# Kernel tuning notes

Measured on AMD Instinct MI355X. Metric: run time of the kernel, lower is better.

Reference implementation:

```python
import jax, jax.numpy as jnp
import numpy as np

C_LIGHT = 3e8
SPATIAL, CROP = 128, 128
BIN_LEN, WALL_SIZE, SAMPLING_COEFF, CYCLES = 0.01, 2.0, 2.0, 5
B, D, T = 1, 2, 96


def waveconvparam(bin_resolution, virtual_wavelength, cycles):
    # Gaussian-windowed virtual cos/sin illumination wave (phasor-field heterodyne).
    s_z = bin_resolution * C_LIGHT
    samples = int(round(cycles * virtual_wavelength / s_z))
    num_cycles = samples * s_z / virtual_wavelength
    sigma = 0.3
    grids_k = np.arange(samples, dtype=np.float64) + 1.0
    sin_wave_k = np.sin(2.0 * np.pi * (num_cycles * grids_k) / samples)
    cos_wave_k = np.cos(2.0 * np.pi * (num_cycles * grids_k) / samples)
    n = np.arange(samples, dtype=np.float64) - (samples - 1) / 2.0
    window = np.exp(-0.5 * (n / (sigma * samples)) ** 2)
    return (cos_wave_k * window).astype(np.float32), (sin_wave_k * window).astype(np.float32)


def definePsf(sptial_grid, temprol_grid, slope):
    # Standard LCT light-cone PSF (O'Toole et al.).
    N, M = sptial_grid, temprol_grid
    x = np.linspace(-1.0, 1.0, 2 * N)
    y = np.linspace(-1.0, 1.0, 2 * N)
    z = np.linspace(0.0, 2.0, 2 * M)
    gz, gy, gx = np.meshgrid(z, y, x, indexing='ij')  # (2M, 2N, 2N)
    psf = np.abs(((4.0 * slope) ** 2) * (gx ** 2 + gy ** 2) - gz)
    psf = (psf == psf.min(axis=0, keepdims=True)).astype(np.float64)
    psf = psf / np.sum(psf[:, N, N])
    psf = psf / np.linalg.norm(psf.ravel())
    psf = np.roll(np.roll(psf, N, axis=1), N, axis=2)
    return psf


def resamplingOperator(M):
    mtx = np.zeros((M * M, M), dtype=np.float64)
    x = np.arange(1, M * M + 1)
    mtx[x - 1, np.ceil(np.sqrt(x)).astype(np.int64) - 1] = 1.0
    mtx = mtx / np.sqrt(x)[:, None]
    mtxi = mtx.T.copy()
    K = int(round(np.log2(M)))
    for _ in range(K):
        mtx = 0.5 * (mtx[0::2] + mtx[1::2])
        mtxi = 0.5 * (mtxi[:, 0::2] + mtxi[:, 1::2])
    return mtx.astype(np.float32), mtxi.astype(np.float32)


def setup_inputs() -> dict:
    key = jax.random.key(0)
    bin_resolution = BIN_LEN / C_LIGHT
    trange = CROP * C_LIGHT * bin_resolution
    width = WALL_SIZE / 2.0
    s_lamda_limit = WALL_SIZE / (SPATIAL - 1)
    virtual_wavelength = SAMPLING_COEFF * (s_lamda_limit * 2.0)
    cosw, sinw = waveconvparam(bin_resolution, virtual_wavelength, CYCLES)
    wave_2xk = np.stack([cosw, sinw], axis=0)[:, ::-1].copy()  # time-reversed, matches module
    psf = definePsf(SPATIAL, CROP, width / trange)
    invpsf = np.conjugate(np.fft.fftn(psf))  # (2*CROP, 2*SPATIAL, 2*SPATIAL)
    mtx, mtxi = resamplingOperator(CROP)
    feat = jax.random.normal(key, (B, D, T, SPATIAL, SPATIAL), dtype=jnp.float32)
    return {
        'feture_bxdxtxhxw': feat,
        'wave_2x1xk': jnp.asarray(wave_2xk[:, None, :], dtype=jnp.float32),
        'mtx_MxM': jnp.asarray(mtx),
        'mtxi_MxM': jnp.asarray(mtxi),
        'invpsf_real': jnp.asarray(np.real(invpsf).astype(np.float32)),
        'invpsf_imag': jnp.asarray(np.imag(invpsf).astype(np.float32)),
        'tbes': jnp.array([16], dtype=jnp.int32),
        'tens': jnp.array([112], dtype=jnp.int32),  # tens = tbes + T, used only via zero-padding
    }


def reference(feture_bxdxtxhxw, wave_2x1xk, mtx_MxM, mtxi_MxM, invpsf_real, invpsf_imag, tbes, tens):
    Bn, Dn, Tn, H, W = feture_bxdxtxhxw.shape
    M = mtx_MxM.shape[0]  # temporal grid (= crop)
    N = H                 # spatial grid
    BD = Bn * Dn

    # --- per-item zero-pad in time to length M (batched, replaces python loop) ---
    def pad_one(x_dthw, tbe):
        z = jnp.zeros((Dn, M, H, W), x_dthw.dtype)
        return jax.lax.dynamic_update_slice(z, x_dthw, (0, tbe, 0, 0))
    data = jax.vmap(pad_one)(feture_bxdxtxhxw, tbes).reshape(BD, M, H, W)

    # --- heterodyne: conv1d along time with reversed cos/sin virtual wave ---
    k = wave_2x1xk.shape[2]
    x = data.transpose(0, 2, 3, 1).reshape(BD * H * W, 1, M)
    y = jax.lax.conv_general_dilated(x, wave_2x1xk, (1,), [(k // 2, k // 2)],
                                     dimension_numbers=('NCH', 'OIH', 'NCH'))
    if k % 2 == 0:
        y = y[:, :, 1:]
    data2 = y.reshape(BD, H, W, 2, M).transpose(3, 0, 4, 1, 2).reshape(2 * BD, M, H, W)

    # --- resampling (LCT warp) ---
    tmp = jnp.einsum('mt,bthw->bmhw', mtx_MxM, data2)

    # --- batched 3D FFT deconvolution with conj(PSF spectrum) ---
    pad = jnp.zeros((2 * BD, 2 * M, 2 * N, 2 * N), tmp.dtype).at[:, :M, :N, :N].set(tmp)
    invpsf = invpsf_real + 1j * invpsf_imag  # complex64, (2M, 2N, 2N)
    vol = jnp.fft.ifftn(jnp.fft.fftn(pad, axes=(1, 2, 3)) * invpsf, axes=(1, 2, 3))[:, :M, :N, :N]

    # --- phasor magnitude: |cos_phasor^2 + sin_phasor^2| combine ---
    sq = vol[:BD] ** 2 + vol[BD:] ** 2  # Re = cr^2-ci^2+sr^2-si^2, Im = 2(cr*ci+sr*si)
    sum_real = jnp.real(sq)
    sum_imag = jnp.imag(sq)
    mag = jnp.sqrt(sum_real ** 2 + sum_imag ** 2)
    sqrt_sum = jnp.sqrt(jax.nn.relu((mag + sum_real) * 0.5))

    # --- inverse resampling ---
    out = jnp.einsum('mt,bthw->bmhw', mtxi_MxM, sqrt_sum)
    return out.reshape(Bn, Dn, M, H, W)
```

## Files before the change

### kernel.cpp

```cpp
#include <hip/hip_runtime.h>
#include <math.h>

typedef float2 c32;

__device__ __forceinline__ c32 cadd(c32 a, c32 b){ return make_float2(a.x+b.x, a.y+b.y); }
__device__ __forceinline__ c32 csub(c32 a, c32 b){ return make_float2(a.x-b.x, a.y-b.y); }
__device__ __forceinline__ c32 cmul(c32 a, c32 b){ return make_float2(fmaf(a.x,b.x,-a.y*b.y), fmaf(a.x,b.y,a.y*b.x)); }
__device__ __forceinline__ c32 cmulc(c32 a, c32 b){ return make_float2(fmaf(a.x,b.x, a.y*b.y), fmaf(a.y,b.x,-a.x*b.y)); }

__device__ __forceinline__ int dr4(int p){
  return ((p&3)<<6) | (((p>>2)&3)<<4) | (((p>>4)&3)<<2) | ((p>>6)&3);
}

template<int S>
__device__ __forceinline__ void dif16(c32 (&z)[16]){
  const float C1=0.92387953251128675613f, S1=0.38268343236508977173f, C2=0.70710678118654752440f;
  const float sg = (float)S;
  const c32 W[8] = { {1.f,0.f},{C1,sg*S1},{C2,sg*C2},{S1,sg*C1},{0.f,sg},{-S1,sg*C1},{-C2,sg*C2},{-C1,sg*S1} };
  #pragma unroll
  for(int j=0;j<8;j++){ c32 a=z[j], b=z[j+8]; z[j]=cadd(a,b); z[j+8]=cmul(csub(a,b), W[j]); }
  #pragma unroll
  for(int blk=0; blk<16; blk+=8){
    #pragma unroll
    for(int j=0;j<4;j++){ c32 a=z[blk+j], b=z[blk+j+4]; z[blk+j]=cadd(a,b); z[blk+j+4]=cmul(csub(a,b), W[2*j]); }
  }
  #pragma unroll
  for(int blk=0; blk<16; blk+=4){
    c32 a=z[blk], b=z[blk+2]; z[blk]=cadd(a,b); z[blk+2]=csub(a,b);
    c32 a1=z[blk+1], b1=z[blk+3]; c32 d=csub(a1,b1);
    z[blk+1]=cadd(a1,b1);
    z[blk+3]= (S<0)? make_float2(d.y,-d.x) : make_float2(-d.y,d.x);
  }
  #pragma unroll
  for(int blk=0; blk<16; blk+=2){ c32 a=z[blk], b=z[blk+1]; z[blk]=cadd(a,b); z[blk+1]=csub(a,b); }
}

template<int S>
__device__ __forceinline__ void dif16_pad(c32 (&z)[16]){
  const float C1=0.92387953251128675613f, S1=0.38268343236508977173f, C2=0.70710678118654752440f;
  const float sg = (float)S;
  const c32 W[8] = { {1.f,0.f},{C1,sg*S1},{C2,sg*C2},{S1,sg*C1},{0.f,sg},{-S1,sg*C1},{-C2,sg*C2},{-C1,sg*S1} };
  z[8]=z[0];
  #pragma unroll
  for(int j=1;j<8;j++) z[j+8]=cmul(z[j], W[j]);
  #pragma unroll
  for(int blk=0; blk<16; blk+=8){
    #pragma unroll
    for(int j=0;j<4;j++){ c32 a=z[blk+j], b=z[blk+j+4]; z[blk+j]=cadd(a,b); z[blk+j+4]=cmul(csub(a,b), W[2*j]); }
  }
  #pragma unroll
  for(int blk=0; blk<16; blk+=4){
    c32 a=z[blk], b=z[blk+2]; z[blk]=cadd(a,b); z[blk+2]=csub(a,b);
    c32 a1=z[blk+1], b1=z[blk+3]; c32 d=csub(a1,b1);
    z[blk+1]=cadd(a1,b1);
    z[blk+3]= (S<0)? make_float2(d.y,-d.x) : make_float2(-d.y,d.x);
  }
  #pragma unroll
  for(int blk=0; blk<16; blk+=2){ c32 a=z[blk], b=z[blk+1]; z[blk]=cadd(a,b); z[blk+1]=csub(a,b); }
}

template<int S>
__device__ __forceinline__ void dif16_crop(c32 (&z)[16]){
  const float C1=0.92387953251128675613f, S1=0.38268343236508977173f, C2=0.70710678118654752440f;
  const float sg = (float)S;
  const c32 W[8] = { {1.f,0.f},{C1,sg*S1},{C2,sg*C2},{S1,sg*C1},{0.f,sg},{-S1,sg*C1},{-C2,sg*C2},{-C1,sg*S1} };
  #pragma unroll
  for(int j=0;j<8;j++){ c32 a=z[j], b=z[j+8]; z[j]=cadd(a,b); z[j+8]=cmul(csub(a,b), W[j]); }
  #pragma unroll
  for(int blk=0; blk<16; blk+=8){
    #pragma unroll
    for(int j=0;j<4;j++){ c32 a=z[blk+j], b=z[blk+j+4]; z[blk+j]=cadd(a,b); z[blk+j+4]=cmul(csub(a,b), W[2*j]); }
  }
  #pragma unroll
  for(int blk=0; blk<16; blk+=4){
    c32 a=z[blk], b=z[blk+2]; z[blk]=cadd(a,b); z[blk+2]=csub(a,b);
    c32 a1=z[blk+1], b1=z[blk+3]; c32 d=csub(a1,b1);
    z[blk+1]=cadd(a1,b1);
    z[blk+3]= (S<0)? make_float2(d.y,-d.x) : make_float2(-d.y,d.x);
  }
  #pragma unroll
  for(int blk=0; blk<16; blk+=2){ z[blk]=cadd(z[blk], z[blk+1]); }
}

__device__ __forceinline__ void dit16(c32 (&z)[16]){
  const float C1=0.92387953251128675613f, S1=0.38268343236508977173f, C2=0.70710678118654752440f;
  const c32 Wc[8] = { {1.f,0.f},{C1,S1},{C2,C2},{S1,C1},{0.f,1.f},{-S1,C1},{-C2,C2},{-C1,S1} };
  #pragma unroll
  for(int p=0;p<16;p+=2){ c32 a=z[p], b=z[p+1]; z[p]=cadd(a,b); z[p+1]=csub(a,b); }
  #pragma unroll
  for(int g=0;g<16;g+=4){
    c32 t=z[g+2]; z[g+2]=csub(z[g],t); z[g]=cadd(z[g],t);
    c32 u=z[g+3]; c32 t1=make_float2(-u.y,u.x); z[g+3]=csub(z[g+1],t1); z[g+1]=cadd(z[g+1],t1);
  }
  #pragma unroll
  for(int g=0;g<16;g+=8){
    #pragma unroll
    for(int j=0;j<4;j++){ c32 t=cmul(z[g+4+j], Wc[2*j]); z[g+4+j]=csub(z[g+j],t); z[g+j]=cadd(z[g+j],t); }
  }
  #pragma unroll
  for(int j=0;j<8;j++){ c32 t=cmul(z[8+j], Wc[j]); z[8+j]=csub(z[j],t); z[j]=cadd(z[j],t); }
}

__launch_bounds__(256)
__global__ void k_setup(const float* __restrict__ mtx, const float* __restrict__ wave,
                        const int* __restrict__ tbes, c32* __restrict__ A, c32* __restrict__ T,
                        int K, int P){
  __shared__ double2 w256[256];
  __shared__ double gre[128];
  __shared__ double gim[128];
  int tid=threadIdx.x; int v=blockIdx.x;
  double ang = -6.2831853071795864769252867665590 * (double)tid / 256.0;
  w256[tid]=make_double2(cos(ang), sin(ang));
  if(v==0) T[tid]=make_float2((float)w256[tid].x,(float)w256[tid].y);
  __syncthreads();
  if(tid<128){
    int tbe=tbes[0];
    double sr=0.0, si=0.0;
    for(int t=0;t<128;t++){
      int jj = v + tbe + P - t;
      if(jj>=0 && jj<K){
        double mv=(double)mtx[tid*128+t];
        sr += mv*(double)wave[jj];
        si += mv*(double)wave[K+jj];
      }
    }
    gre[tid]=sr; gim[tid]=si;
  }
  __syncthreads();
  double ar=0.0, ai=0.0;
  int k=tid;
  for(int m=0;m<128;m++){
    double2 f=w256[(k*m)&255];
    ar += f.x*gre[m] - f.y*gim[m];
    ai += f.x*gim[m] + f.y*gre[m];
  }
  A[(long)dr4(k)*96 + v] = make_float2((float)ar,(float)ai);
}

__launch_bounds__(256)
__global__ void k_front(const float* __restrict__ feat, const c32* __restrict__ A, c32* __restrict__ buf){
  __shared__ __align__(16) float Xs[48*128];
  __shared__ __align__(16) c32 As[64*48];
  int tid=threadIdx.x; int b=blockIdx.x;
  int d=b>>9, h=(b>>2)&127, kb=(b&3)*64;
  c32 acc[8][4];
  #pragma unroll
  for(int i=0;i<8;i++){
    #pragma unroll
    for(int j=0;j<4;j++) acc[i][j]=make_float2(0.f,0.f);
  }
  int kg=tid>>5, wg=tid&31;
  for(int vc=0; vc<2; vc++){
    #pragma unroll
    for(int i=0;i<6;i++){
      int idx=tid+i*256;
      int v=idx>>5, w4=idx&31;
      *(float4*)&Xs[v*128 + w4*4] = *(const float4*)&feat[(((long)d*96 + vc*48+v)*128 + h)*128 + w4*4];
    }
    #pragma unroll
    for(int i=0;i<6;i++){
      int idx=tid+i*256;
      int kk=idx/24, rem=idx-kk*24;
      *(float4*)&As[kk*48 + rem*2] = *(const float4*)&A[(long)(kb+kk)*96 + vc*48 + rem*2];
    }
    __syncthreads();
    #pragma unroll 4
    for(int vv=0; vv<48; vv++){
      float4 xv = *(const float4*)&Xs[vv*128 + wg*4];
      #pragma unroll
      for(int i=0;i<8;i++){
        c32 a = As[(kg*8+i)*48 + vv];
        acc[i][0].x = fmaf(a.x, xv.x, acc[i][0].x); acc[i][0].y = fmaf(a.y, xv.x, acc[i][0].y);
        acc[i][1].x = fmaf(a.x, xv.y, acc[i][1].x); acc[i][1].y = fmaf(a.y, xv.y, acc[i][1].y);
        acc[i][2].x = fmaf(a.x, xv.z, acc[i][2].x); acc[i][2].y = fmaf(a.y, xv.z, acc[i][2].y);
        acc[i][3].x = fmaf(a.x, xv.w, acc[i][3].x); acc[i][3].y = fmaf(a.y, xv.w, acc[i][3].y);
      }
    }
    __syncthreads();
  }
  #pragma unroll
  for(int i=0;i<8;i++){
    int k=kb+kg*8+i;
    long o = (((long)d*256 + k)*256 + h)*128 + wg*4;
    *(float4*)&buf[o]   = make_float4(acc[i][0].x,acc[i][0].y,acc[i][1].x,acc[i][1].y);
    *(float4*)&buf[o+2] = make_float4(acc[i][2].x,acc[i][2].y,acc[i][3].x,acc[i][3].y);
  }
}

__launch_bounds__(256)
__global__ void k_ffty(c32* __restrict__ buf, const c32* __restrict__ T){
  __shared__ c32 tile[256*17];
  __shared__ c32 Ts[256];
  int tid=threadIdx.x;
  Ts[tid]=T[tid];
  int b=blockIdx.x;
  int d=b>>11, k=(b>>3)&255, w0=(b&7)*16;
  long base = (((long)d*256 + k)*256)*128 + w0;
  __syncthreads();
  #pragma unroll
  for(int it=0; it<4; it++){
    int idx = tid + it*256; int w = idx&15, j = idx>>4;
    c32 x0 = buf[base + (long)j*128 + w];
    c32 x1 = buf[base + (long)(j+64)*128 + w];
    tile[j*17+w] = cadd(x0,x1);
    c32 y1 = make_float2(x0.x + x1.y, x0.y - x1.x);
    c32 y2 = csub(x0,x1);
    c32 y3 = make_float2(x0.x - x1.y, x0.y + x1.x);
    tile[(j+64)*17+w]  = cmul(y1, Ts[j]);
    tile[(j+128)*17+w] = cmul(y2, Ts[(2*j)&255]);
    tile[(j+192)*17+w] = cmul(y3, Ts[(3*j)&255]);
  }
  __syncthreads();
  #pragma unroll
  for(int s=1;s<4;s++){
    int quarter = 64 >> (2*s);
    int m4 = quarter<<2;
    int sh = 2*s;
    #pragma unroll
    for(int it=0;it<4;it++){
      int idx=tid+it*256; int w=idx&15, bf=idx>>4;
      int g = bf/quarter, j = bf - g*quarter;
      int p0 = g*m4 + j;
      c32 x0=tile[p0*17+w], x1=tile[(p0+quarter)*17+w], x2=tile[(p0+2*quarter)*17+w], x3=tile[(p0+3*quarter)*17+w];
      c32 t0=cadd(x0,x2), t1=csub(x0,x2), t2=cadd(x1,x3), t3=csub(x1,x3);
      c32 y0=cadd(t0,t2);
      c32 y2=csub(t0,t2);
      c32 y1=make_float2(t1.x + t3.y, t1.y - t3.x);
      c32 y3=make_float2(t1.x - t3.y, t1.y + t3.x);
      tile[p0*17+w]=y0;
      tile[(p0+quarter)*17+w]  =cmul(y1, Ts[(j<<sh)&255]);
      tile[(p0+2*quarter)*17+w]=cmul(y2, Ts[((2*j)<<sh)&255]);
      tile[(p0+3*quarter)*17+w]=cmul(y3, Ts[((3*j)<<sh)&255]);
    }
    __syncthreads();
  }
  #pragma unroll
  for(int it=0;it<16;it++){
    int idx=tid+it*256; int w=idx&15, p=idx>>4;
    buf[base + (long)p*128 + w] = tile[p*17+w];
  }
}

__launch_bounds__(256)
__global__ void k_fftx(c32* __restrict__ buf, const float* __restrict__ pre,
                       const float* __restrict__ pim, const c32* __restrict__ T){
  __shared__ c32 tile[16*276];
  __shared__ c32 Ts[256];
  const int BR[16]={0,8,4,12,2,10,6,14,1,9,5,13,3,11,7,15};
  int tid=threadIdx.x;
  Ts[tid]=T[tid];
  int lane = tid & 63;
  int L = ((tid>>6)<<2) + (lane>>4);
  int n1 = lane & 15;
  int k = blockIdx.x >> 5;
  int q = ((blockIdx.x & 31)<<3) + (L & 7);
  int d = L >> 3;
  long lbase = (((long)d*256 + k)*256 + q)*128;
  long prow = (((long)dr4(k))*256 + dr4(q))*256;
  c32* tl = &tile[L*276];
  const float* pb_re = pre + prow + n1;
  const float* pb_im = pim + prow + n1;
  c32 h[16];
  #pragma unroll
  for(int r=0;r<16;r++){ h[r].x = pb_re[16*BR[r]]; h[r].y = pb_im[16*BR[r]]; }
  c32 z[16];
  #pragma unroll
  for(int r=0;r<8;r++) z[r] = buf[lbase + n1 + 16*r];
  __syncthreads();
  dif16_pad<-1>(z);
  #pragma unroll
  for(int r=1;r<16;r++) z[r] = cmul(z[r], Ts[(n1*BR[r])&255]);
  #pragma unroll
  for(int r=0;r<16;r++) tl[BR[r]*17 + n1] = z[r];
  __builtin_amdgcn_wave_barrier();
  #pragma unroll
  for(int c=0;c<16;c++) z[c] = tl[n1*17 + c];
  dif16<-1>(z);
  #pragma unroll
  for(int r=0;r<16;r++) z[r] = cmul(z[r], h[r]);
  dit16(z);
  #pragma unroll
  for(int r=1;r<16;r++) z[r] = cmulc(z[r], Ts[(r*n1)&255]);
  __builtin_amdgcn_wave_barrier();
  #pragma unroll
  for(int r=0;r<16;r++) tl[r*17 + n1] = z[r];
  __builtin_amdgcn_wave_barrier();
  #pragma unroll
  for(int c=0;c<16;c++) z[c] = tl[n1*17 + c];
  dif16_crop<1>(z);
  const float s = 1.f/256.f;
  #pragma unroll
  for(int r=0;r<16;r+=2){
    int n2 = BR[r];
    buf[lbase + n1 + 16*n2] = make_float2(z[r].x*s, z[r].y*s);
  }
}

__launch_bounds__(256)
__global__ void k_iffty(c32* __restrict__ buf, const c32* __restrict__ T){
  __shared__ c32 tile[256*17];
  __shared__ c32 Ts[256];
  int tid=threadIdx.x;
  Ts[tid]=T[tid];
  int b=blockIdx.x;
  int d=b>>11, k=(b>>3)&255, x0=(b&7)*16;
  long base = (((long)d*256 + k)*256)*128 + x0;
  __syncthreads();
  #pragma unroll
  for(int it=0;it<16;it++){
    int idx=tid+it*256; int w=idx&15, p=idx>>4;
    tile[p*17+w]=buf[base + (long)p*128 + w];
  }
  __syncthreads();
  #pragma unroll
  for(int s=0;s<3;s++){
    int quarter = 1<<(2*s);
    int m4 = quarter<<2;
    int sh = 2*(3-s);
    #pragma unroll
    for(int it=0;it<4;it++){
      int idx=tid+it*256; int w=idx&15, bf=idx>>4;
      int g=bf/quarter, j=bf-g*quarter;
      int p0=g*m4+j;
      c32 t0=tile[p0*17+w];
      c32 t1=cmulc(tile[(p0+quarter)*17+w],   Ts[(j<<sh)&255]);
      c32 t2=cmulc(tile[(p0+2*quarter)*17+w], Ts[((2*j)<<sh)&255]);
      c32 t3=cmulc(tile[(p0+3*quarter)*17+w], Ts[((3*j)<<sh)&255]);
      c32 y0 = make_float2(t0.x+t1.x+t2.x+t3.x, t0.y+t1.y+t2.y+t3.y);
      c32 y1 = make_float2(t0.x - t1.y - t2.x + t3.y, t0.y + t1.x - t2.y - t3.x);
      c32 y2 = make_float2(t0.x - t1.x + t2.x - t3.x, t0.y - t1.y + t2.y - t3.y);
      c32 y3 = make_float2(t0.x + t1.y - t2.x - t3.y, t0.y - t1.x - t2.y + t3.x);
      tile[p0*17+w]=y0; tile[(p0+quarter)*17+w]=y1; tile[(p0+2*quarter)*17+w]=y2; tile[(p0+3*quarter)*17+w]=y3;
    }
    __syncthreads();
  }
  const float sc = 1.f/256.f;
  #pragma unroll
  for(int it=0;it<4;it++){
    int idx=tid+it*256; int w=idx&15, j=idx>>4;
    c32 t0=tile[j*17+w];
    c32 t1=cmulc(tile[(j+64)*17+w],  Ts[j]);
    c32 t2=cmulc(tile[(j+128)*17+w], Ts[(2*j)&255]);
    c32 t3=cmulc(tile[(j+192)*17+w], Ts[(3*j)&255]);
    c32 y0 = make_float2((t0.x+t1.x+t2.x+t3.x)*sc, (t0.y+t1.y+t2.y+t3.y)*sc);
    c32 y1 = make_float2((t0.x - t1.y - t2.x + t3.y)*sc, (t0.y + t1.x - t2.y - t3.x)*sc);
    buf[base + (long)j*128 + w] = y0;
    buf[base + (long)(j+64)*128 + w] = y1;
  }
}

__launch_bounds__(256)
__global__ void k_back(c32* __restrict__ buf, const float* __restrict__ mtxi,
                       const c32* __restrict__ T, float* __restrict__ out){
  __shared__ c32 tile[256*17];
  __shared__ float magl[128*16];
  __shared__ c32 Ts[256];
  int tid=threadIdx.x;
  Ts[tid]=T[tid];
  int b=blockIdx.x;
  int d=b>>10, y=(b>>3)&127, x0=(b&7)*16;
  __syncthreads();
  #pragma unroll
  for(int it=0;it<16;it++){
    int idx=tid+it*256; int w=idx&15, p=idx>>4;
    tile[p*17+w]=buf[(((long)d*256 + p)*256 + y)*128 + x0 + w];
  }
  __syncthreads();
  #pragma unroll
  for(int s=0;s<3;s++){
    int quarter = 1<<(2*s);
    int m4 = quarter<<2;
    int sh = 2*(3-s);
    #pragma unroll
    for(int it=0;it<4;it++){
      int idx=tid+it*256; int w=idx&15, bf=idx>>4;
      int g=bf/quarter, j=bf-g*quarter;
      int p0=g*m4+j;
      c32 t0=tile[p0*17+w];
      c32 t1=cmulc(tile[(p0+quarter)*17+w],   Ts[(j<<sh)&255]);
      c32 t2=cmulc(tile[(p0+2*quarter)*17+w], Ts[((2*j)<<sh)&255]);
      c32 t3=cmulc(tile[(p0+3*quarter)*17+w], Ts[((3*j)<<sh)&255]);
      c32 y0 = make_float2(t0.x+t1.x+t2.x+t3.x, t0.y+t1.y+t2.y+t3.y);
      c32 y1 = make_float2(t0.x - t1.y - t2.x + t3.y, t0.y + t1.x - t2.y - t3.x);
      c32 y2 = make_float2(t0.x - t1.x + t2.x - t3.x, t0.y - t1.y + t2.y - t3.y);
      c32 y3 = make_float2(t0.x + t1.y - t2.x - t3.y, t0.y - t1.x - t2.y + t3.x);
      tile[p0*17+w]=y0; tile[(p0+quarter)*17+w]=y1; tile[(p0+2*quarter)*17+w]=y2; tile[(p0+3*quarter)*17+w]=y3;
    }
    __syncthreads();
  }
  const float sc = 1.f/256.f;
  #pragma unroll
  for(int it=0;it<4;it++){
    int idx=tid+it*256; int w=idx&15, j=idx>>4;
    c32 t0=tile[j*17+w];
    c32 t1=cmulc(tile[(j+64)*17+w],  Ts[j]);
    c32 t2=cmulc(tile[(j+128)*17+w], Ts[(2*j)&255]);
    c32 t3=cmulc(tile[(j+192)*17+w], Ts[(3*j)&255]);
    float y0r = t0.x+t1.x+t2.x+t3.x, y0i = t0.y+t1.y+t2.y+t3.y;
    float y1r = t0.x - t1.y - t2.x + t3.y, y1i = t0.y + t1.x - t2.y - t3.x;
    magl[j*16 + w]      = sqrtf(y0r*y0r + y0i*y0i) * sc;
    magl[(j+64)*16 + w] = sqrtf(y1r*y1r + y1i*y1i) * sc;
  }
  __syncthreads();
  float* mt = (float*)tile;
  int xg = tid&3, mg = tid>>2;
  #pragma unroll
  for(int c=0;c<2;c++){
    #pragma unroll
    for(int it=0;it<32;it++){
      int idx=tid+it*256; int t=idx&127, mm=idx>>7;
      mt[t*68+mm] = mtxi[(c*64+mm)*128 + t];
    }
    __syncthreads();
    float4 a = make_float4(0.f,0.f,0.f,0.f);
    #pragma unroll 4
    for(int t=0;t<128;t++){
      float mv = mt[t*68 + mg];
      float4 g = *(const float4*)&magl[t*16 + xg*4];
      a.x = fmaf(mv, g.x, a.x); a.y = fmaf(mv, g.y, a.y);
      a.z = fmaf(mv, g.z, a.z); a.w = fmaf(mv, g.w, a.w);
    }
    int m_ = c*64 + mg;
    *(float4*)&out[(((long)d*128 + m_)*128 + y)*128 + x0 + xg*4] = a;
    __syncthreads();
  }
}

extern "C" void kernel_launch(void* const* d_in, const int* in_sizes, int n_in,
                              void* d_out, int out_size, void* d_ws, size_t ws_size,
                              hipStream_t stream) {
  const float* feat=(const float*)d_in[0];
  const float* wave=(const float*)d_in[1];
  const float* mtx =(const float*)d_in[2];
  const float* mtxi=(const float*)d_in[3];
  const float* pre =(const float*)d_in[4];
  const float* pim =(const float*)d_in[5];
  const int*   tbes=(const int*)d_in[6];
  float* out=(float*)d_out;
  char* ws=(char*)d_ws;
  c32* A   = (c32*)ws;
  c32* T   = (c32*)(ws + 196608);
  c32* buf = (c32*)(ws + 262144);

  int K = in_sizes[1] / 2;
  int P = (K & 1) ? (K/2) : (K/2 - 1);

  hipLaunchKernelGGL(k_setup, dim3(96),   dim3(256), 0, stream, mtx, wave, tbes, A, T, K, P);
  hipLaunchKernelGGL(k_front, dim3(1024), dim3(256), 0, stream, feat, A, buf);
  hipLaunchKernelGGL(k_ffty,  dim3(4096), dim3(256), 0, stream, buf, T);
  hipLaunchKernelGGL(k_fftx,  dim3(8192), dim3(256), 0, stream, buf, pre, pim, T);
  hipLaunchKernelGGL(k_iffty, dim3(4096), dim3(256), 0, stream, buf, T);
  hipLaunchKernelGGL(k_back,  dim3(2048), dim3(256), 0, stream, buf, mtxi, T, out);
}
```

Baseline: 251.8 us.

## Use nontemporal IO, split re/im LDS, and swizzle block order in x-FFT kernel

The x-axis FFT/PSF-multiply kernel now loads and stores its working buffer with nontemporal hints and stores the LDS transpose tile as separate real and imaginary float arrays to cut bank conflicts. The block index is remapped so that consecutive blocks spread across k-slices, and an asm barrier pins the PSF loads early. Wave barriers are replaced with full block __syncthreads, which adds synchronisation cost. The gain depends on cache and LDS behaviour.

```diff
diff --git a/kernel.cpp b/kernel.cpp
--- a/kernel.cpp
+++ b/kernel.cpp
@@ -7,6 +7,16 @@
 __device__ __forceinline__ c32 csub(c32 a, c32 b){ return make_float2(a.x-b.x, a.y-b.y); }
 __device__ __forceinline__ c32 cmul(c32 a, c32 b){ return make_float2(fmaf(a.x,b.x,-a.y*b.y), fmaf(a.x,b.y,a.y*b.x)); }
 __device__ __forceinline__ c32 cmulc(c32 a, c32 b){ return make_float2(fmaf(a.x,b.x, a.y*b.y), fmaf(a.y,b.x,-a.x*b.y)); }
+
+__device__ __forceinline__ c32 ntload(const c32* p){
+  double v = __builtin_nontemporal_load(reinterpret_cast<const double*>(p));
+  union { double d; float f[2]; } u; u.d = v;
+  return make_float2(u.f[0], u.f[1]);
+}
+__device__ __forceinline__ void ntstore(c32* p, c32 v){
+  union { double d; float f[2]; } u; u.f[0]=v.x; u.f[1]=v.y;
+  __builtin_nontemporal_store(u.d, reinterpret_cast<double*>(p));
+}
 
 __device__ __forceinline__ int dr4(int p){
   return ((p&3)<<6) | (((p>>2)&3)<<4) | (((p>>4)&3)<<2) | ((p>>6)&3);
@@ -244,7 +254,8 @@
 __launch_bounds__(256)
 __global__ void k_fftx(c32* __restrict__ buf, const float* __restrict__ pre,
                        const float* __restrict__ pim, const c32* __restrict__ T){
-  __shared__ c32 tile[16*276];
+  __shared__ float lre[16*272];
+  __shared__ float lim[16*272];
   __shared__ c32 Ts[256];
   const int BR[16]={0,8,4,12,2,10,6,14,1,9,5,13,3,11,7,15};
   int tid=threadIdx.x;
@@ -252,12 +263,14 @@
   int lane = tid & 63;
   int L = ((tid>>6)<<2) + (lane>>4);
   int n1 = lane & 15;
-  int k = blockIdx.x >> 5;
-  int q = ((blockIdx.x & 31)<<3) + (L & 7);
+  int b = blockIdx.x;
+  int bs = ((b & 7) << 10) | (b >> 3);
+  int k = bs >> 5;
+  int q = ((bs & 31)<<3) + (L & 7);
   int d = L >> 3;
   long lbase = (((long)d*256 + k)*256 + q)*128;
   long prow = (((long)dr4(k))*256 + dr4(q))*256;
-  c32* tl = &tile[L*276];
+  int Lb = L*272;
   const float* pb_re = pre + prow + n1;
   const float* pb_im = pim + prow + n1;
   c32 h[16];
@@ -265,34 +278,36 @@
   for(int r=0;r<16;r++){ h[r].x = pb_re[16*BR[r]]; h[r].y = pb_im[16*BR[r]]; }
   c32 z[16];
   #pragma unroll
-  for(int r=0;r<8;r++) z[r] = buf[lbase + n1 + 16*r];
+  for(int r=0;r<8;r++) z[r] = ntload(&buf[lbase + n1 + 16*r]);
+  #pragma unroll
+  for(int r=0;r<16;r++){ asm volatile("" : "+v"(h[r].x), "+v"(h[r].y)); }
   __syncthreads();
   dif16_pad<-1>(z);
   #pragma unroll
   for(int r=1;r<16;r++) z[r] = cmul(z[r], Ts[(n1*BR[r])&255]);
   #pragma unroll
-  for(int r=0;r<16;r++) tl[BR[r]*17 + n1] = z[r];
-  __builtin_amdgcn_wave_barrier();
-  #pragma unroll
-  for(int c=0;c<16;c++) z[c] = tl[n1*17 + c];
+  for(int r=0;r<16;r++){ int o = Lb + BR[r]*17 + n1; lre[o]=z[r].x; lim[o]=z[r].y; }
+  __syncthreads();
+  #pragma unroll
+  for(int c=0;c<16;c++){ int o = Lb + n1*17 + c; z[c]=make_float2(lre[o], lim[o]); }
   dif16<-1>(z);
   #pragma unroll
   for(int r=0;r<16;r++) z[r] = cmul(z[r], h[r]);
   dit16(z);
   #pragma unroll
   for(int r=1;r<16;r++) z[r] = cmulc(z[r], Ts[(r*n1)&255]);
-  __builtin_amdgcn_wave_barrier();
-  #pragma unroll
-  for(int r=0;r<16;r++) tl[r*17 + n1] = z[r];
-  __builtin_amdgcn_wave_barrier();
-  #pragma unroll
-  for(int c=0;c<16;c++) z[c] = tl[n1*17 + c];
+  __syncthreads();
+  #pragma unroll
+  for(int r=0;r<16;r++){ int o = Lb + r*17 + n1; lre[o]=z[r].x; lim[o]=z[r].y; }
+  __syncthreads();
+  #pragma unroll
+  for(int c=0;c<16;c++){ int o = Lb + n1*17 + c; z[c]=make_float2(lre[o], lim[o]); }
   dif16_crop<1>(z);
   const float s = 1.f/256.f;
   #pragma unroll
   for(int r=0;r<16;r+=2){
     int n2 = BR[r];
-    buf[lbase + n1 + 16*n2] = make_float2(z[r].x*s, z[r].y*s);
+    ntstore(&buf[lbase + n1 + 16*n2], make_float2(z[r].x*s, z[r].y*s));
   }
 }
 
```

Result: no change. 247.8 us (-1.6%).
